# Performance work log

Hardware: AMD Instinct MI355X
Metric: run time of the kernel (lower is better)

## Reference

```python
import jax, jax.numpy as jnp
import numpy as np

HID = 64
NUM_LAYER = 3
N_OBJ = 100000
N_P1, N_P2, N_P3 = 200000, 400000, 200000
NUM_GRAPHS = 256


def _mlp(x, w1, b1, w2, b2):
    # pyg.nn.MLP([in, hid, out], norm=None): Linear -> ReLU -> Linear
    return jnp.dot(jax.nn.relu(jnp.dot(x, w1) + b1), w2) + b2


def _gather(obj, ei):
    # ei: [arity, n_atoms] object index per argument slot
    r, n = ei.shape
    g = jnp.take(obj, ei, axis=0)  # [r, n, HID]
    return jnp.moveaxis(g, 0, 1).reshape(n, r * HID)  # concat per-position embeddings


def _scatter(atom, ei, n_obj):
    # split atom embedding [n, r*HID] into r chunks and scatter-add to objects
    r, n = ei.shape
    chunks = jnp.moveaxis(atom.reshape(n, r, HID), 1, 0).reshape(r * n, HID)
    return jax.ops.segment_sum(chunks, ei.reshape(-1), num_segments=n_obj)


def _lin_init(key, fan_in, fan_out):
    kw, kb = jax.random.split(key)
    w = jax.random.normal(kw, (fan_in, fan_out), jnp.float32) / np.float32(np.sqrt(fan_in))
    b = jax.random.normal(kb, (fan_out,), jnp.float32) * 0.01
    return w, b


def setup_inputs() -> dict:
    key = jax.random.key(0)
    ks = jax.random.split(key, 16)
    inp = {}
    inp["x_obj"] = jnp.zeros((N_OBJ, 1), jnp.float32)
    inp["x_p1"] = jnp.zeros((N_P1, 1), jnp.float32)
    inp["x_p2"] = jnp.zeros((N_P2, 2), jnp.float32)
    inp["x_p3"] = jnp.zeros((N_P3, 3), jnp.float32)
    for i, (name, r) in enumerate([("p1", 1), ("p2", 2), ("p3", 3)]):
        d = HID * r
        w1, b1 = _lin_init(ks[2 * i], d, d)
        w2, b2 = _lin_init(ks[2 * i + 1], d, d)
        inp[f"w_{name}_1"], inp[f"b_{name}_1"] = w1, b1
        inp[f"w_{name}_2"], inp[f"b_{name}_2"] = w2, b2
    inp["w_u1"], inp["b_u1"] = _lin_init(ks[6], 2 * HID, 2 * HID)
    inp["w_u2"], inp["b_u2"] = _lin_init(ks[7], 2 * HID, HID)
    inp["w_r1"], inp["b_r1"] = _lin_init(ks[8], HID, 2 * HID)
    inp["w_r2"], inp["b_r2"] = _lin_init(ks[9], 2 * HID, 1)
    inp["ei_p1"] = jax.random.randint(ks[10], (1, N_P1), 0, N_OBJ, jnp.int32)
    inp["ei_p2"] = jax.random.randint(ks[11], (2, N_P2), 0, N_OBJ, jnp.int32)
    inp["ei_p3"] = jax.random.randint(ks[12], (3, N_P3), 0, N_OBJ, jnp.int32)
    inp["batch_obj"] = jnp.sort(jax.random.randint(ks[13], (N_OBJ,), 0, NUM_GRAPHS, jnp.int32))
    inp["num_graphs"] = NUM_GRAPHS
    return inp


def reference(x_obj, x_p1, x_p2, x_p3,
              w_p1_1, b_p1_1, w_p1_2, b_p1_2,
              w_p2_1, b_p2_1, w_p2_2, b_p2_2,
              w_p3_1, b_p3_1, w_p3_2, b_p3_2,
              w_u1, b_u1, w_u2, b_u2,
              w_r1, b_r1, w_r2, b_r2,
              ei_p1, ei_p2, ei_p3, batch_obj, num_graphs):
    n_obj = x_obj.shape[0]
    # encoding_layer: everything starts at zeros of size [N, F*hidden]
    obj = jnp.zeros((n_obj, x_obj.shape[1] * HID), jnp.float32)
    for _ in range(NUM_LAYER):
        # FanOutMP: gather arg-object embeddings, per-predicate MLP -> atom embeddings
        a1 = _mlp(_gather(obj, ei_p1), w_p1_1, b_p1_1, w_p1_2, b_p1_2)
        a2 = _mlp(_gather(obj, ei_p2), w_p2_1, b_p2_1, w_p2_2, b_p2_2)
        a3 = _mlp(_gather(obj, ei_p3), w_p3_1, b_p3_1, w_p3_2, b_p3_2)
        # FanInMP: split atom emb into arity chunks, scatter-add back to objects
        agg = (_scatter(a1, ei_p1, n_obj) + _scatter(a2, ei_p2, n_obj)
               + _scatter(a3, ei_p3, n_obj))
        # obj_update on cat([old_obj, aggregated])
        obj = _mlp(jnp.concatenate([obj, agg], axis=1), w_u1, b_u1, w_u2, b_u2)
    # global_add_pool + readout
    pooled = jax.ops.segment_sum(obj, batch_obj, num_segments=num_graphs)
    return _mlp(pooled, w_r1, b_r1, w_r2, b_r2).reshape(-1)
```

## Files before the change

### kernel.cpp

```cpp
#include <hip/hip_runtime.h>

typedef _Float16 h8 __attribute__((ext_vector_type(8)));
typedef float f32x4 __attribute__((ext_vector_type(4)));

__device__ __forceinline__ f32x4 mfma2(h8 ah, h8 bh, h8 bl, f32x4 c) {
    c = __builtin_amdgcn_mfma_f32_16x16x32_f16(ah, bh, c, 0, 0, 0);
    c = __builtin_amdgcn_mfma_f32_16x16x32_f16(ah, bl, c, 0, 0, 0);
    return c;
}

__launch_bounds__(256)
__global__ void wprep(const float* __restrict__ w_p1_1, const float* __restrict__ w_p1_2,
                      const float* __restrict__ w_p2_1, const float* __restrict__ w_p2_2,
                      const float* __restrict__ w_p3_1, const float* __restrict__ w_p3_2,
                      const float* __restrict__ w_u1, const float* __restrict__ w_u2,
                      _Float16* __restrict__ hb)
{
    int b = blockIdx.x;
    const float* src; int K, N, base; size_t off;
    if      (b < 16)  { src = w_p1_1; K = 64;  N = 64;  base = 0;   off = 0;      }
    else if (b < 32)  { src = w_p1_2; K = 64;  N = 64;  base = 16;  off = 8192;   }
    else if (b < 96)  { src = w_p2_1; K = 128; N = 128; base = 32;  off = 16384;  }
    else if (b < 160) { src = w_p2_2; K = 128; N = 128; base = 96;  off = 49152;  }
    else if (b < 304) { src = w_p3_1; K = 192; N = 192; base = 160; off = 81920;  }
    else if (b < 448) { src = w_p3_2; K = 192; N = 192; base = 304; off = 155648; }
    else if (b < 512) { src = w_u1;   K = 128; N = 128; base = 448; off = 229376; }
    else              { src = w_u2;   K = 128; N = 64;  base = 512; off = 262144; }
    int e = (b - base) * 256 + threadIdx.x;
    if (e < K * N) {
        int n = e / K, k = e - n * K;
        float x = src[k * N + n];
        _Float16 h = (_Float16)x;
        hb[off + e] = h;
        hb[off + (size_t)K * N + e] = (_Float16)(x - (float)h);
    }
}

__launch_bounds__(256)
__global__ void aconst_k(const float* __restrict__ b_p1_1, const float* __restrict__ w_p1_2,
                         const float* __restrict__ b_p1_2,
                         const float* __restrict__ b_p2_1, const float* __restrict__ w_p2_2,
                         const float* __restrict__ b_p2_2,
                         const float* __restrict__ b_p3_1, const float* __restrict__ w_p3_2,
                         const float* __restrict__ b_p3_2,
                         float* __restrict__ ac)
{
    int p = blockIdx.x;
    const float *b1, *w2, *b2; int D, off;
    if      (p == 0) { b1 = b_p1_1; w2 = w_p1_2; b2 = b_p1_2; D = 64;  off = 0;   }
    else if (p == 1) { b1 = b_p2_1; w2 = w_p2_2; b2 = b_p2_2; D = 128; off = 64;  }
    else             { b1 = b_p3_1; w2 = w_p3_2; b2 = b_p3_2; D = 192; off = 192; }
    int n = threadIdx.x;
    if (n < D) {
        float s = b2[n];
        for (int k = 0; k < D; ++k) {
            float h = b1[k];
            h = h > 0.f ? h : 0.f;
            s = fmaf(h, w2[k * D + n], s);
        }
        ac[off + n] = s;
    }
}

__launch_bounds__(256)
__global__ void hist_k(const int* __restrict__ ei1, const int* __restrict__ ei2,
                       const int* __restrict__ ei3, int* __restrict__ counts,
                       int n_obj, int n1, int n2, int n3)
{
    int e = blockIdx.x * 256 + threadIdx.x;
    int t1 = n1, t2 = n1 + 2 * n2, t3 = t2 + 3 * n3;
    int o, j;
    if (e < t1) { o = ei1[e]; j = 0; }
    else if (e < t2) { int x = e - t1; o = ei2[x]; j = 1 + (x >= n2 ? 1 : 0); }
    else if (e < t3) { int y = e - t2; o = ei3[y]; j = 3 + (y >= n3 ? 1 : 0) + (y >= 2 * n3 ? 1 : 0); }
    else return;
    atomicAdd(&counts[(size_t)j * n_obj + o], 1);
    atomicAdd(&counts[(size_t)6 * n_obj + o], 1);
}

__launch_bounds__(1024)
__global__ void scan_k(const int* __restrict__ deg, int* __restrict__ rowptr,
                       int* __restrict__ cursor, int n)
{
    __shared__ int buf[1024];
    __shared__ int carry_s;
    int tid = threadIdx.x;
    if (tid == 0) carry_s = 0;
    __syncthreads();
    for (int base = 0; base < n; base += 4096) {
        int idx = base + tid * 4;
        int v[4];
#pragma unroll
        for (int k = 0; k < 4; ++k) { int i = idx + k; v[k] = (i < n) ? deg[i] : 0; }
        int tsum = v[0] + v[1] + v[2] + v[3];
        buf[tid] = tsum;
        __syncthreads();
        for (int off = 1; off < 1024; off <<= 1) {
            int t = (tid >= off) ? buf[tid - off] : 0;
            __syncthreads();
            buf[tid] += t;
            __syncthreads();
        }
        int run = buf[tid] - tsum + carry_s;
#pragma unroll
        for (int k = 0; k < 4; ++k) {
            int i = idx + k;
            if (i < n) { rowptr[i] = run; cursor[i] = run; }
            run += v[k];
        }
        __syncthreads();
        if (tid == 1023) carry_s += buf[1023];
        __syncthreads();
    }
    if (tid == 0) rowptr[n] = carry_s;
}

__launch_bounds__(256)
__global__ void fill_k(const int* __restrict__ ei1, const int* __restrict__ ei2,
                       const int* __restrict__ ei3, int* __restrict__ cursor,
                       int* __restrict__ colidx, int n1, int n2, int n3)
{
    int e = blockIdx.x * 256 + threadIdx.x;
    int t1 = n1, t2 = n1 + 2 * n2, t3 = t2 + 3 * n3;
    int o;
    if (e < t1) o = ei1[e];
    else if (e < t2) o = ei2[e - t1];
    else if (e < t3) o = ei3[e - t2];
    else return;
    int pos = atomicAdd(&cursor[o], 1);
    colidx[pos] = e;
}

__launch_bounds__(256)
__global__ void bcast_k(const int* __restrict__ counts, const float* __restrict__ ac,
                        float* __restrict__ agg, int n_obj)
{
    __shared__ float ch[384];
    int tid = threadIdx.x;
    for (int i = tid; i < 384; i += 256) ch[i] = ac[i];
    __syncthreads();
    int i = blockIdx.x * 256 + tid;
    int o = i >> 4, q = i & 15;
    if (o < n_obj) {
        float c[6];
#pragma unroll
        for (int j = 0; j < 6; ++j) c[j] = (float)counts[(size_t)j * n_obj + o];
        float4 v;
        float* vp = (float*)&v;
#pragma unroll
        for (int comp = 0; comp < 4; ++comp) {
            int col = 4 * q + comp;
            float s = 0.f;
#pragma unroll
            for (int j = 0; j < 6; ++j) s = fmaf(c[j], ch[j * 64 + col], s);
            vp[comp] = s;
        }
        ((float4*)agg)[(size_t)o * 16 + q] = v;
    }
}

template<int R, int STORE>
__device__ __forceinline__ void pred_body(
    char* smem,
    const _Float16* __restrict__ objh, const int* __restrict__ ei,
    const _Float16* __restrict__ W1h, const _Float16* __restrict__ W1l,
    const float* __restrict__ B1,
    const _Float16* __restrict__ W2h, const _Float16* __restrict__ W2l,
    const float* __restrict__ B2,
    float* __restrict__ agg, _Float16* __restrict__ chunks, int cbase,
    int n_atoms, int blk)
{
    constexpr int D = 64 * R;
    constexpr int KC = D / 32;
    constexpr int LDA = D + 8;
    _Float16* Ah = (_Float16*)smem;
    int* eis = (int*)(Ah + 64 * LDA);

    const int tid = threadIdx.x;
    const int wave = tid >> 6, lane = tid & 63;
    const int r = lane & 15, g = lane >> 4;
    const int a_base = blk * 64;
    const int tb = wave * R;

    for (int i = tid; i < R * 64; i += 256) {
        int s = i >> 6, a = i & 63;
        int ag = a_base + a; if (ag >= n_atoms) ag = n_atoms - 1;
        eis[i] = ei[s * n_atoms + ag];
    }
    __syncthreads();
    {
        h8 vv[2 * R];
#pragma unroll
        for (int i = 0; i < 2 * R; ++i) {
            int f = tid + 256 * i;
            int rowslot = f >> 3, c = f & 7;
            int s = rowslot >> 6, a = rowslot & 63;
            vv[i] = *(const h8*)(objh + (size_t)eis[s * 64 + a] * 64 + c * 8);
        }
#pragma unroll
        for (int i = 0; i < 2 * R; ++i) {
            int f = tid + 256 * i;
            int rowslot = f >> 3, c = f & 7;
            int s = rowslot >> 6, a = rowslot & 63;
            *(h8*)(Ah + a * LDA + s * 64 + c * 8) = vv[i];
        }
    }
    __syncthreads();

    f32x4 z = {0.f, 0.f, 0.f, 0.f};
    f32x4 acc[4][R];
#pragma unroll
    for (int rt = 0; rt < 4; ++rt)
#pragma unroll
        for (int t = 0; t < R; ++t) acc[rt][t] = z;

    {
        h8 bh[2][R], bl[2][R];
#pragma unroll
        for (int t = 0; t < R; ++t) {
            size_t wo = (size_t)((tb + t) * 16 + r) * D + g * 8;
            bh[0][t] = *(const h8*)(W1h + wo);
            bl[0][t] = *(const h8*)(W1l + wo);
        }
#pragma unroll
        for (int kc = 0; kc < KC; ++kc) {
            const int cur = kc & 1, nxt = cur ^ 1;
            if (kc + 1 < KC) {
#pragma unroll
                for (int t = 0; t < R; ++t) {
                    size_t wo = (size_t)((tb + t) * 16 + r) * D + (kc + 1) * 32 + g * 8;
                    bh[nxt][t] = *(const h8*)(W1h + wo);
                    bl[nxt][t] = *(const h8*)(W1l + wo);
                }
            }
            const int ko = kc * 32 + g * 8;
            h8 ah[4];
#pragma unroll
            for (int rt = 0; rt < 4; ++rt)
                ah[rt] = *(const h8*)(Ah + (rt * 16 + r) * LDA + ko);
#pragma unroll
            for (int t = 0; t < R; ++t)
#pragma unroll
                for (int rt = 0; rt < 4; ++rt)
                    acc[rt][t] = mfma2(ah[rt], bh[cur][t], bl[cur][t], acc[rt][t]);
        }
    }
    __syncthreads();
#pragma unroll
    for (int t = 0; t < R; ++t) {
        int col = (tb + t) * 16 + r;
        float b1 = B1[col];
#pragma unroll
        for (int rt = 0; rt < 4; ++rt)
#pragma unroll
            for (int q = 0; q < 4; ++q) {
                int row = rt * 16 + g * 4 + q;
                float h = acc[rt][t][q] + b1;
                h = h > 0.f ? h : 0.f;
                Ah[row * LDA + col] = (_Float16)h;
            }
    }
    __syncthreads();

#pragma unroll
    for (int rt = 0; rt < 4; ++rt)
#pragma unroll
        for (int t = 0; t < R; ++t) acc[rt][t] = z;
    {
        h8 bh[2][R], bl[2][R];
#pragma unroll
        for (int t = 0; t < R; ++t) {
            size_t wo = (size_t)((tb + t) * 16 + r) * D + g * 8;
            bh[0][t] = *(const h8*)(W2h + wo);
            bl[0][t] = *(const h8*)(W2l + wo);
        }
#pragma unroll
        for (int kc = 0; kc < KC; ++kc) {
            const int cur = kc & 1, nxt = cur ^ 1;
            if (kc + 1 < KC) {
#pragma unroll
                for (int t = 0; t < R; ++t) {
                    size_t wo = (size_t)((tb + t) * 16 + r) * D + (kc + 1) * 32 + g * 8;
                    bh[nxt][t] = *(const h8*)(W2h + wo);
                    bl[nxt][t] = *(const h8*)(W2l + wo);
                }
            }
            const int ko = kc * 32 + g * 8;
            h8 ah[4];
#pragma unroll
            for (int rt = 0; rt < 4; ++rt)
                ah[rt] = *(const h8*)(Ah + (rt * 16 + r) * LDA + ko);
#pragma unroll
            for (int t = 0; t < R; ++t)
#pragma unroll
                for (int rt = 0; rt < 4; ++rt)
                    acc[rt][t] = mfma2(ah[rt], bh[cur][t], bl[cur][t], acc[rt][t]);
        }
    }

#pragma unroll
    for (int t = 0; t < R; ++t) {
        int col = (tb + t) * 16 + r;
        float b2 = B2[col];
        int s = col >> 6, cc = col & 63;
#pragma unroll
        for (int rt = 0; rt < 4; ++rt)
#pragma unroll
            for (int q = 0; q < 4; ++q) {
                int row = rt * 16 + g * 4 + q;
                int atom = a_base + row;
                if (atom < n_atoms) {
                    float v = acc[rt][t][q] + b2;
                    if (STORE) {
                        chunks[(size_t)(cbase + s * n_atoms + atom) * 64 + cc] = (_Float16)v;
                    } else {
                        atomicAdd(agg + (size_t)eis[s * 64 + row] * 64 + cc, v);
                    }
                }
            }
    }
}

template<int STORE>
__launch_bounds__(256, 6)
__global__ void pred_all(const _Float16* __restrict__ objh, float* __restrict__ agg,
                         _Float16* __restrict__ chunks,
                         const int* __restrict__ ei1, const int* __restrict__ ei2,
                         const int* __restrict__ ei3,
                         const _Float16* __restrict__ hb,
                         const float* __restrict__ b_p1_1, const float* __restrict__ b_p1_2,
                         const float* __restrict__ b_p2_1, const float* __restrict__ b_p2_2,
                         const float* __restrict__ b_p3_1, const float* __restrict__ b_p3_2,
                         int n1, int n2, int n3, int nb3, int nb2)
{
    extern __shared__ char smem[];
    int b = blockIdx.x;
    if (b < nb3) {
        pred_body<3, STORE>(smem, objh, ei3, hb + 81920, hb + 118784, b_p3_1,
                            hb + 155648, hb + 192512, b_p3_2, agg, chunks,
                            n1 + 2 * n2, n3, b);
    } else if (b < nb3 + nb2) {
        pred_body<2, STORE>(smem, objh, ei2, hb + 16384, hb + 32768, b_p2_1,
                            hb + 49152, hb + 65536, b_p2_2, agg, chunks,
                            n1, n2, b - nb3);
    } else {
        pred_body<1, STORE>(smem, objh, ei1, hb + 0, hb + 4096, b_p1_1,
                            hb + 8192, hb + 12288, b_p1_2, agg, chunks,
                            0, n1, b - nb3 - nb2);
    }
}

__launch_bounds__(256, 4)
__global__ void fanin_update(_Float16* __restrict__ objh,
                             const _Float16* __restrict__ chunks,
                             const int* __restrict__ rowptr, const int* __restrict__ colidx,
                             const _Float16* __restrict__ W1h, const _Float16* __restrict__ W1l,
                             const float* __restrict__ B1,
                             const _Float16* __restrict__ W2h, const _Float16* __restrict__ W2l,
                             const float* __restrict__ B2,
                             int n_obj, int last, float* __restrict__ aggout)
{
    constexpr int LDA = 136;
    __shared__ _Float16 Ah[64 * LDA];
    __shared__ int cidx[2048];

    const int tid = threadIdx.x;
    const int wave = tid >> 6, lane = tid & 63;
    const int r = lane & 15, g = lane >> 4;
    const int a_base = blockIdx.x * 64;
    const int o_hi = (a_base + 64 < n_obj) ? a_base + 64 : n_obj;

    const int sbeg = rowptr[a_base];
    const int send = rowptr[o_hi];
    const int total = send - sbeg;
    const int ncache = total < 2048 ? total : 2048;
    for (int i = tid; i < ncache; i += 256) cidx[i] = colidx[sbeg + i];

    const int o_local = tid >> 2, part = tid & 3;
    const int o = a_base + o_local;
    const bool valid = o < n_obj;
    const int b = valid ? rowptr[o] : 0;
    const int e2 = valid ? rowptr[o + 1] : 0;
    float s[16];
#pragma unroll
    for (int j = 0; j < 16; ++j) s[j] = 0.f;
    __syncthreads();
    for (int i = b; i < e2; ++i) {
        int li = i - sbeg;
        int row = (li < ncache) ? cidx[li] : colidx[i];
        const h8* cp = (const h8*)(chunks + (size_t)row * 64 + part * 16);
        h8 v0 = cp[0], v1 = cp[1];
#pragma unroll
        for (int j = 0; j < 8; ++j) { s[j] += (float)v0[j]; s[8 + j] += (float)v1[j]; }
    }
    {
        int oc = valid ? o : n_obj - 1;
        h8 u0 = *(const h8*)(objh + (size_t)oc * 64 + part * 16);
        h8 u1 = *(const h8*)(objh + (size_t)oc * 64 + part * 16 + 8);
        *(h8*)(Ah + o_local * LDA + part * 16) = u0;
        *(h8*)(Ah + o_local * LDA + part * 16 + 8) = u1;
        h8 a0, a1;
#pragma unroll
        for (int j = 0; j < 8; ++j) { a0[j] = (_Float16)s[j]; a1[j] = (_Float16)s[8 + j]; }
        *(h8*)(Ah + o_local * LDA + 64 + part * 16) = a0;
        *(h8*)(Ah + o_local * LDA + 64 + part * 16 + 8) = a1;
    }
    __syncthreads();

    f32x4 z = {0.f, 0.f, 0.f, 0.f};
    f32x4 acc[4][2];
#pragma unroll
    for (int rt = 0; rt < 4; ++rt) { acc[rt][0] = z; acc[rt][1] = z; }
    {
        h8 bh[2][2], bl[2][2];
#pragma unroll
        for (int t = 0; t < 2; ++t) {
            size_t wo = (size_t)((wave * 2 + t) * 16 + r) * 128 + g * 8;
            bh[0][t] = *(const h8*)(W1h + wo);
            bl[0][t] = *(const h8*)(W1l + wo);
        }
#pragma unroll
        for (int kc = 0; kc < 4; ++kc) {
            const int cur = kc & 1, nxt = cur ^ 1;
            if (kc + 1 < 4) {
#pragma unroll
                for (int t = 0; t < 2; ++t) {
                    size_t wo = (size_t)((wave * 2 + t) * 16 + r) * 128 + (kc + 1) * 32 + g * 8;
                    bh[nxt][t] = *(const h8*)(W1h + wo);
                    bl[nxt][t] = *(const h8*)(W1l + wo);
                }
            }
            const int ko = kc * 32 + g * 8;
            h8 ah[4];
#pragma unroll
            for (int rt = 0; rt < 4; ++rt)
                ah[rt] = *(const h8*)(Ah + (rt * 16 + r) * LDA + ko);
#pragma unroll
            for (int t = 0; t < 2; ++t)
#pragma unroll
                for (int rt = 0; rt < 4; ++rt)
                    acc[rt][t] = mfma2(ah[rt], bh[cur][t], bl[cur][t], acc[rt][t]);
        }
    }
    __syncthreads();
#pragma unroll
    for (int t = 0; t < 2; ++t) {
        int col = (wave * 2 + t) * 16 + r;
        float b1 = B1[col];
#pragma unroll
        for (int rt = 0; rt < 4; ++rt)
#pragma unroll
            for (int q = 0; q < 4; ++q) {
                int row = rt * 16 + g * 4 + q;
                float h = acc[rt][t][q] + b1;
                h = h > 0.f ? h : 0.f;
                Ah[row * LDA + col] = (_Float16)h;
            }
    }
    __syncthreads();

    f32x4 acc2[4];
#pragma unroll
    for (int rt = 0; rt < 4; ++rt) acc2[rt] = z;
    {
        h8 bh[2], bl[2];
        {
            size_t wo = (size_t)(wave * 16 + r) * 128 + g * 8;
            bh[0] = *(const h8*)(W2h + wo);
            bl[0] = *(const h8*)(W2l + wo);
        }
#pragma unroll
        for (int kc = 0; kc < 4; ++kc) {
            const int cur = kc & 1, nxt = cur ^ 1;
            if (kc + 1 < 4) {
                size_t wo = (size_t)(wave * 16 + r) * 128 + (kc + 1) * 32 + g * 8;
                bh[nxt] = *(const h8*)(W2h + wo);
                bl[nxt] = *(const h8*)(W2l + wo);
            }
            const int ko = kc * 32 + g * 8;
#pragma unroll
            for (int rt = 0; rt < 4; ++rt) {
                h8 ah = *(const h8*)(Ah + (rt * 16 + r) * LDA + ko);
                acc2[rt] = mfma2(ah, bh[cur], bl[cur], acc2[rt]);
            }
        }
    }
    {
        int col = wave * 16 + r;
        float b2 = B2[col];
#pragma unroll
        for (int rt = 0; rt < 4; ++rt)
#pragma unroll
            for (int q = 0; q < 4; ++q) {
                int row = a_base + rt * 16 + g * 4 + q;
                if (row < n_obj) {
                    float v = acc2[rt][q] + b2;
                    if (last) aggout[(size_t)row * 64 + col] = v;
                    else objh[(size_t)row * 64 + col] = (_Float16)v;
                }
            }
    }
}

template<int FIRST>
__launch_bounds__(256, 4)
__global__ void update_mfma(_Float16* __restrict__ objh, float* __restrict__ agg,
                            const _Float16* __restrict__ W1h, const _Float16* __restrict__ W1l,
                            const float* __restrict__ B1,
                            const _Float16* __restrict__ W2h, const _Float16* __restrict__ W2l,
                            const float* __restrict__ B2,
                            int n_obj, int zero_agg, int last)
{
    constexpr int LDA = 136;
    __shared__ _Float16 Ah[64 * LDA];

    const int tid = threadIdx.x;
    const int wave = tid >> 6, lane = tid & 63;
    const int r = lane & 15, g = lane >> 4;
    const int a_base = blockIdx.x * 64;

    {
#pragma unroll
        for (int i = 0; i < 4; ++i) {
            int f = tid + 256 * i;
            int a = f >> 4, c = f & 15;
            int rg = a_base + a; if (rg >= n_obj) rg = n_obj - 1;
            h8 v;
            if (c < 8) {
                if (FIRST) v = (h8)(_Float16)0.f;
                else v = *(const h8*)(objh + (size_t)rg * 64 + c * 8);
            } else {
                float4 f0 = ((const float4*)agg)[(size_t)rg * 16 + (c - 8) * 2];
                float4 f1 = ((const float4*)agg)[(size_t)rg * 16 + (c - 8) * 2 + 1];
                v[0] = (_Float16)f0.x; v[1] = (_Float16)f0.y;
                v[2] = (_Float16)f0.z; v[3] = (_Float16)f0.w;
                v[4] = (_Float16)f1.x; v[5] = (_Float16)f1.y;
                v[6] = (_Float16)f1.z; v[7] = (_Float16)f1.w;
            }
            *(h8*)(Ah + a * LDA + c * 8) = v;
        }
    }
    __syncthreads();

    f32x4 z = {0.f, 0.f, 0.f, 0.f};
    f32x4 acc[4][2];
#pragma unroll
    for (int rt = 0; rt < 4; ++rt) { acc[rt][0] = z; acc[rt][1] = z; }
    {
        h8 bh[2][2], bl[2][2];
#pragma unroll
        for (int t = 0; t < 2; ++t) {
            size_t wo = (size_t)((wave * 2 + t) * 16 + r) * 128 + g * 8;
            bh[0][t] = *(const h8*)(W1h + wo);
            bl[0][t] = *(const h8*)(W1l + wo);
        }
#pragma unroll
        for (int kc = 0; kc < 4; ++kc) {
            const int cur = kc & 1, nxt = cur ^ 1;
            if (kc + 1 < 4) {
#pragma unroll
                for (int t = 0; t < 2; ++t) {
                    size_t wo = (size_t)((wave * 2 + t) * 16 + r) * 128 + (kc + 1) * 32 + g * 8;
                    bh[nxt][t] = *(const h8*)(W1h + wo);
                    bl[nxt][t] = *(const h8*)(W1l + wo);
                }
            }
            const int ko = kc * 32 + g * 8;
            h8 ah[4];
#pragma unroll
            for (int rt = 0; rt < 4; ++rt)
                ah[rt] = *(const h8*)(Ah + (rt * 16 + r) * LDA + ko);
#pragma unroll
            for (int t = 0; t < 2; ++t)
#pragma unroll
                for (int rt = 0; rt < 4; ++rt)
                    acc[rt][t] = mfma2(ah[rt], bh[cur][t], bl[cur][t], acc[rt][t]);
        }
    }
    __syncthreads();
#pragma unroll
    for (int t = 0; t < 2; ++t) {
        int col = (wave * 2 + t) * 16 + r;
        float b1 = B1[col];
#pragma unroll
        for (int rt = 0; rt < 4; ++rt)
#pragma unroll
            for (int q = 0; q < 4; ++q) {
                int row = rt * 16 + g * 4 + q;
                float h = acc[rt][t][q] + b1;
                h = h > 0.f ? h : 0.f;
                Ah[row * LDA + col] = (_Float16)h;
            }
    }
    __syncthreads();

    f32x4 acc2[4];
#pragma unroll
    for (int rt = 0; rt < 4; ++rt) acc2[rt] = z;
    {
        h8 bh[2], bl[2];
        {
            size_t wo = (size_t)(wave * 16 + r) * 128 + g * 8;
            bh[0] = *(const h8*)(W2h + wo);
            bl[0] = *(const h8*)(W2l + wo);
        }
#pragma unroll
        for (int kc = 0; kc < 4; ++kc) {
            const int cur = kc & 1, nxt = cur ^ 1;
            if (kc + 1 < 4) {
                size_t wo = (size_t)(wave * 16 + r) * 128 + (kc + 1) * 32 + g * 8;
                bh[nxt] = *(const h8*)(W2h + wo);
                bl[nxt] = *(const h8*)(W2l + wo);
            }
            const int ko = kc * 32 + g * 8;
#pragma unroll
            for (int rt = 0; rt < 4; ++rt) {
                h8 ah = *(const h8*)(Ah + (rt * 16 + r) * LDA + ko);
                acc2[rt] = mfma2(ah, bh[cur], bl[cur], acc2[rt]);
            }
        }
    }
    __syncthreads();
    {
        int col = wave * 16 + r;
        float b2 = B2[col];
#pragma unroll
        for (int rt = 0; rt < 4; ++rt)
#pragma unroll
            for (int q = 0; q < 4; ++q) {
                int row = a_base + rt * 16 + g * 4 + q;
                if (row < n_obj) {
                    float v = acc2[rt][q] + b2;
                    if (last) agg[(size_t)row * 64 + col] = v;
                    else objh[(size_t)row * 64 + col] = (_Float16)v;
                }
            }
    }
    if (zero_agg) {
        float4 zz = make_float4(0.f, 0.f, 0.f, 0.f);
#pragma unroll
        for (int i = 0; i < 4; ++i) {
            int f = tid + 256 * i;
            int a = f >> 4, q = f & 15;
            int rg = a_base + a;
            if (rg < n_obj) ((float4*)agg)[(size_t)rg * 16 + q] = zz;
        }
    }
}

__global__ void pool_kernel(const float* __restrict__ obj, const int* __restrict__ batch,
                            float* __restrict__ pooled, int n_obj)
{
    int i = blockIdx.x * 256 + threadIdx.x;
    int row = i >> 4, q = i & 15;
    if (row < n_obj) {
        float4 v = ((const float4*)obj)[(size_t)row * 16 + q];
        int g = batch[row];
        float* p = pooled + g * 64 + 4 * q;
        atomicAdd(p + 0, v.x);
        atomicAdd(p + 1, v.y);
        atomicAdd(p + 2, v.z);
        atomicAdd(p + 3, v.w);
    }
}

__launch_bounds__(128)
__global__ void readout_kernel(const float* __restrict__ pooled,
                               const float* __restrict__ w1, const float* __restrict__ b1,
                               const float* __restrict__ w2, const float* __restrict__ b2,
                               float* __restrict__ out)
{
    int g = blockIdx.x, c = threadIdx.x;
    __shared__ float xs[64];
    __shared__ float red[2];
    if (c < 64) xs[c] = pooled[g * 64 + c];
    __syncthreads();
    float h = b1[c];
#pragma unroll
    for (int k = 0; k < 64; ++k) h = fmaf(xs[k], w1[k * 128 + c], h);
    float v = fmaxf(h, 0.f) * w2[c];
#pragma unroll
    for (int off = 32; off > 0; off >>= 1) v += __shfl_down(v, off);
    if ((c & 63) == 0) red[c >> 6] = v;
    __syncthreads();
    if (c == 0) out[g] = red[0] + red[1] + b2[0];
}

static inline size_t align_up(size_t x) { return (x + 255) & ~(size_t)255; }

extern "C" void kernel_launch(void* const* d_in, const int* in_sizes, int n_in,
                              void* d_out, int out_size, void* d_ws, size_t ws_size,
                              hipStream_t stream)
{
    const float* w_p1_1 = (const float*)d_in[4];
    const float* b_p1_1 = (const float*)d_in[5];
    const float* w_p1_2 = (const float*)d_in[6];
    const float* b_p1_2 = (const float*)d_in[7];
    const float* w_p2_1 = (const float*)d_in[8];
    const float* b_p2_1 = (const float*)d_in[9];
    const float* w_p2_2 = (const float*)d_in[10];
    const float* b_p2_2 = (const float*)d_in[11];
    const float* w_p3_1 = (const float*)d_in[12];
    const float* b_p3_1 = (const float*)d_in[13];
    const float* w_p3_2 = (const float*)d_in[14];
    const float* b_p3_2 = (const float*)d_in[15];
    const float* w_u1 = (const float*)d_in[16];
    const float* b_u1 = (const float*)d_in[17];
    const float* w_u2 = (const float*)d_in[18];
    const float* b_u2 = (const float*)d_in[19];
    const float* w_r1 = (const float*)d_in[20];
    const float* b_r1 = (const float*)d_in[21];
    const float* w_r2 = (const float*)d_in[22];
    const float* b_r2 = (const float*)d_in[23];
    const int* ei_p1 = (const int*)d_in[24];
    const int* ei_p2 = (const int*)d_in[25];
    const int* ei_p3 = (const int*)d_in[26];
    const int* batch = (const int*)d_in[27];

    const int n_obj = in_sizes[0];
    const int n_p1 = in_sizes[24];
    const int n_p2 = in_sizes[25] / 2;
    const int n_p3 = in_sizes[26] / 3;
    const int E = n_p1 + 2 * n_p2 + 3 * n_p3;

    char* base = (char*)d_ws;
    size_t off = 0;
    _Float16* objh = (_Float16*)(base + off); off = align_up(off + (size_t)n_obj * 64 * 2);
    float* agg = (float*)(base + off);        off = align_up(off + (size_t)n_obj * 64 * 4);
    float* pooled = (float*)(base + off);     off = align_up(off + (size_t)out_size * 64 * 4);
    _Float16* hb = (_Float16*)(base + off);   off = align_up(off + (size_t)278528 * 2);
    int* counts = (int*)(base + off);         off = align_up(off + (size_t)7 * n_obj * 4);
    int* deg = counts + (size_t)6 * n_obj;
    int* rowptr = (int*)(base + off);         off = align_up(off + ((size_t)n_obj + 1) * 4);
    int* cursor = (int*)(base + off);         off = align_up(off + (size_t)n_obj * 4);
    int* colidx = (int*)(base + off);         off = align_up(off + (size_t)E * 4);
    _Float16* chunks = (_Float16*)(base + off); off = align_up(off + (size_t)E * 64 * 2);
    const bool csr_ok = off <= ws_size;

    const int nb3 = (n_p3 + 63) / 64, nb2 = (n_p2 + 63) / 64, nb1 = (n_p1 + 63) / 64;
    const int pred_smem = 64 * (192 + 8) * 2 + 3 * 64 * 4;

    wprep<<<544, 256, 0, stream>>>(w_p1_1, w_p1_2, w_p2_1, w_p2_2, w_p3_1, w_p3_2,
                                   w_u1, w_u2, hb);
    aconst_k<<<3, 256, 0, stream>>>(b_p1_1, w_p1_2, b_p1_2, b_p2_1, w_p2_2, b_p2_2,
                                    b_p3_1, w_p3_2, b_p3_2, agg);
    float* ac = pooled;
    aconst_k<<<3, 256, 0, stream>>>(b_p1_1, w_p1_2, b_p1_2, b_p2_1, w_p2_2, b_p2_2,
                                    b_p3_1, w_p3_2, b_p3_2, ac);
    hipMemsetAsync(counts, 0, (size_t)7 * n_obj * sizeof(int), stream);
    hist_k<<<(E + 255) / 256, 256, 0, stream>>>(ei_p1, ei_p2, ei_p3, counts,
                                                n_obj, n_p1, n_p2, n_p3);
    if (csr_ok) {
        scan_k<<<1, 1024, 0, stream>>>(deg, rowptr, cursor, n_obj);
        fill_k<<<(E + 255) / 256, 256, 0, stream>>>(ei_p1, ei_p2, ei_p3, cursor, colidx,
                                                    n_p1, n_p2, n_p3);
    }
    bcast_k<<<((size_t)n_obj * 16 + 255) / 256, 256, 0, stream>>>(counts, ac, agg, n_obj);
    update_mfma<1><<<(n_obj + 63) / 64, 256, 0, stream>>>(
        objh, agg, hb + 229376, hb + 245760, b_u1, hb + 262144, hb + 270336, b_u2,
        n_obj, csr_ok ? 0 : 1, 0);
    if (csr_ok) {
        for (int l = 1; l < 3; ++l) {
            pred_all<1><<<nb3 + nb2 + nb1, 256, pred_smem, stream>>>(
                objh, agg, chunks, ei_p1, ei_p2, ei_p3, hb,
                b_p1_1, b_p1_2, b_p2_1, b_p2_2, b_p3_1, b_p3_2,
                n_p1, n_p2, n_p3, nb3, nb2);
            fanin_update<<<(n_obj + 63) / 64, 256, 0, stream>>>(
                objh, chunks, rowptr, colidx,
                hb + 229376, hb + 245760, b_u1, hb + 262144, hb + 270336, b_u2,
                n_obj, l == 2 ? 1 : 0, agg);
        }
    } else {
        for (int l = 1; l < 3; ++l) {
            pred_all<0><<<nb3 + nb2 + nb1, 256, pred_smem, stream>>>(
                objh, agg, chunks, ei_p1, ei_p2, ei_p3, hb,
                b_p1_1, b_p1_2, b_p2_1, b_p2_2, b_p3_1, b_p3_2,
                n_p1, n_p2, n_p3, nb3, nb2);
            update_mfma<0><<<(n_obj + 63) / 64, 256, 0, stream>>>(
                objh, agg, hb + 229376, hb + 245760, b_u1, hb + 262144, hb + 270336, b_u2,
                n_obj, l < 2 ? 1 : 0, l == 2 ? 1 : 0);
        }
    }
    hipMemsetAsync(pooled, 0, (size_t)out_size * 64 * sizeof(float), stream);
    pool_kernel<<<((size_t)n_obj * 16 + 255) / 256, 256, 0, stream>>>(agg, batch, pooled, n_obj);
    readout_kernel<<<out_size, 128, 0, stream>>>(pooled, w_r1, b_r1, w_r2, b_r2, (float*)d_out);
}
```

Before: 1.469 ms.

## Scatter atom chunks directly into CSR order and store aggregate in fp16

fill_k now records each edge's destination slot in the CSR order. The predicate kernel stages its outputs in shared memory and writes each 64-wide chunk straight to that slot, so fanin_update reads contiguous chunks with no colidx indirection or index caching. The aggregate buffer becomes fp16, with half2 atomics in the fallback path and h8 loads in the update kernel, which halves traffic. In exchange, the chunk writes become scattered and extra syncthreads are added, and fp16 accumulation in the fallback loses precision.

```diff
diff --git a/kernel.cpp b/kernel.cpp
--- a/kernel.cpp
+++ b/kernel.cpp
@@ -1,4 +1,5 @@
 #include <hip/hip_runtime.h>
+#include <hip/hip_fp16.h>
 
 typedef _Float16 h8 __attribute__((ext_vector_type(8)));
 typedef float f32x4 __attribute__((ext_vector_type(4)));
@@ -118,7 +119,7 @@
 __launch_bounds__(256)
 __global__ void fill_k(const int* __restrict__ ei1, const int* __restrict__ ei2,
                        const int* __restrict__ ei3, int* __restrict__ cursor,
-                       int* __restrict__ colidx, int n1, int n2, int n3)
+                       int* __restrict__ epos, int n1, int n2, int n3)
 {
     int e = blockIdx.x * 256 + threadIdx.x;
     int t1 = n1, t2 = n1 + 2 * n2, t3 = t2 + 3 * n3;
@@ -127,35 +128,33 @@
     else if (e < t2) o = ei2[e - t1];
     else if (e < t3) o = ei3[e - t2];
     else return;
-    int pos = atomicAdd(&cursor[o], 1);
-    colidx[pos] = e;
+    epos[e] = atomicAdd(&cursor[o], 1);
 }
 
 __launch_bounds__(256)
 __global__ void bcast_k(const int* __restrict__ counts, const float* __restrict__ ac,
-                        float* __restrict__ agg, int n_obj)
+                        _Float16* __restrict__ aggh, int n_obj)
 {
     __shared__ float ch[384];
     int tid = threadIdx.x;
     for (int i = tid; i < 384; i += 256) ch[i] = ac[i];
     __syncthreads();
     int i = blockIdx.x * 256 + tid;
-    int o = i >> 4, q = i & 15;
+    int o = i >> 3, q = i & 7;
     if (o < n_obj) {
         float c[6];
 #pragma unroll
         for (int j = 0; j < 6; ++j) c[j] = (float)counts[(size_t)j * n_obj + o];
-        float4 v;
-        float* vp = (float*)&v;
-#pragma unroll
-        for (int comp = 0; comp < 4; ++comp) {
-            int col = 4 * q + comp;
+        h8 v;
+#pragma unroll
+        for (int comp = 0; comp < 8; ++comp) {
+            int col = 8 * q + comp;
             float s = 0.f;
 #pragma unroll
             for (int j = 0; j < 6; ++j) s = fmaf(c[j], ch[j * 64 + col], s);
-            vp[comp] = s;
-        }
-        ((float4*)agg)[(size_t)o * 16 + q] = v;
+            v[comp] = (_Float16)s;
+        }
+        *(h8*)(aggh + (size_t)o * 64 + 8 * q) = v;
     }
 }
 
@@ -163,11 +162,12 @@
 __device__ __forceinline__ void pred_body(
     char* smem,
     const _Float16* __restrict__ objh, const int* __restrict__ ei,
+    const int* __restrict__ epos, int cbase,
     const _Float16* __restrict__ W1h, const _Float16* __restrict__ W1l,
     const float* __restrict__ B1,
     const _Float16* __restrict__ W2h, const _Float16* __restrict__ W2l,
     const float* __restrict__ B2,
-    float* __restrict__ agg, _Float16* __restrict__ chunks, int cbase,
+    _Float16* __restrict__ aggh, _Float16* __restrict__ chunks,
     int n_atoms, int blk)
 {
     constexpr int D = 64 * R;
@@ -298,33 +298,61 @@
         }
     }
 
-#pragma unroll
-    for (int t = 0; t < R; ++t) {
-        int col = (tb + t) * 16 + r;
-        float b2 = B2[col];
-        int s = col >> 6, cc = col & 63;
-#pragma unroll
-        for (int rt = 0; rt < 4; ++rt)
-#pragma unroll
-            for (int q = 0; q < 4; ++q) {
-                int row = rt * 16 + g * 4 + q;
-                int atom = a_base + row;
-                if (atom < n_atoms) {
+    if (STORE) {
+        __syncthreads();
+#pragma unroll
+        for (int t = 0; t < R; ++t) {
+            int col = (tb + t) * 16 + r;
+            float b2 = B2[col];
+            int s = col >> 6, cc = col & 63;
+#pragma unroll
+            for (int rt = 0; rt < 4; ++rt)
+#pragma unroll
+                for (int q = 0; q < 4; ++q) {
+                    int row = rt * 16 + g * 4 + q;
+                    Ah[row * LDA + s * 64 + cc] = (_Float16)(acc[rt][t][q] + b2);
+                }
+        }
+        __syncthreads();
+#pragma unroll
+        for (int p = 0; p < 2 * R; ++p) {
+            int i = p * 32 + (tid >> 3);
+            int s = i >> 6, a = i & 63;
+            int c8 = tid & 7;
+            int atom = a_base + a;
+            if (atom < n_atoms) {
+                int pos = epos[cbase + s * n_atoms + atom];
+                *(h8*)(chunks + (size_t)pos * 64 + c8 * 8) =
+                    *(const h8*)(Ah + a * LDA + s * 64 + c8 * 8);
+            }
+        }
+    } else {
+#pragma unroll
+        for (int t = 0; t < R; ++t) {
+            int col = (tb + t) * 16 + r;
+            float b2 = B2[col];
+            int s = col >> 6, cc = col & 63;
+#pragma unroll
+            for (int rt = 0; rt < 4; ++rt)
+#pragma unroll
+                for (int q = 0; q < 4; ++q) {
+                    int row = rt * 16 + g * 4 + q;
+                    int atom = a_base + row;
                     float v = acc[rt][t][q] + b2;
-                    if (STORE) {
-                        chunks[(size_t)(cbase + s * n_atoms + atom) * 64 + cc] = (_Float16)v;
-                    } else {
-                        atomicAdd(agg + (size_t)eis[s * 64 + row] * 64 + cc, v);
+                    float v2 = __shfl_xor(v, 1);
+                    if (atom < n_atoms && (r & 1) == 0) {
+                        __half2 hv = __floats2half2_rn(v, v2);
+                        unsafeAtomicAdd((__half2*)(aggh + (size_t)eis[s * 64 + row] * 64 + cc), hv);
                     }
                 }
-            }
+        }
     }
 }
 
 template<int STORE>
 __launch_bounds__(256, 6)
-__global__ void pred_all(const _Float16* __restrict__ objh, float* __restrict__ agg,
-                         _Float16* __restrict__ chunks,
+__global__ void pred_all(const _Float16* __restrict__ objh, _Float16* __restrict__ aggh,
+                         _Float16* __restrict__ chunks, const int* __restrict__ epos,
                          const int* __restrict__ ei1, const int* __restrict__ ei2,
                          const int* __restrict__ ei3,
                          const _Float16* __restrict__ hb,
@@ -336,45 +364,37 @@
     extern __shared__ char smem[];
     int b = blockIdx.x;
     if (b < nb3) {
-        pred_body<3, STORE>(smem, objh, ei3, hb + 81920, hb + 118784, b_p3_1,
-                            hb + 155648, hb + 192512, b_p3_2, agg, chunks,
-                            n1 + 2 * n2, n3, b);
+        pred_body<3, STORE>(smem, objh, ei3, epos, n1 + 2 * n2,
+                            hb + 81920, hb + 118784, b_p3_1,
+                            hb + 155648, hb + 192512, b_p3_2, aggh, chunks, n3, b);
     } else if (b < nb3 + nb2) {
-        pred_body<2, STORE>(smem, objh, ei2, hb + 16384, hb + 32768, b_p2_1,
-                            hb + 49152, hb + 65536, b_p2_2, agg, chunks,
-                            n1, n2, b - nb3);
+        pred_body<2, STORE>(smem, objh, ei2, epos, n1,
+                            hb + 16384, hb + 32768, b_p2_1,
+                            hb + 49152, hb + 65536, b_p2_2, aggh, chunks, n2, b - nb3);
     } else {
-        pred_body<1, STORE>(smem, objh, ei1, hb + 0, hb + 4096, b_p1_1,
-                            hb + 8192, hb + 12288, b_p1_2, agg, chunks,
-                            0, n1, b - nb3 - nb2);
+        pred_body<1, STORE>(smem, objh, ei1, epos, 0,
+                            hb + 0, hb + 4096, b_p1_1,
+                            hb + 8192, hb + 12288, b_p1_2, aggh, chunks, n1, b - nb3 - nb2);
     }
 }
 
 __launch_bounds__(256, 4)
 __global__ void fanin_update(_Float16* __restrict__ objh,
                              const _Float16* __restrict__ chunks,
-                             const int* __restrict__ rowptr, const int* __restrict__ colidx,
+                             const int* __restrict__ rowptr,
                              const _Float16* __restrict__ W1h, const _Float16* __restrict__ W1l,
                              const float* __restrict__ B1,
                              const _Float16* __restrict__ W2h, const _Float16* __restrict__ W2l,
                              const float* __restrict__ B2,
-                             int n_obj, int last, float* __restrict__ aggout)
+                             int n_obj, int last, float* __restrict__ aggf)
 {
     constexpr int LDA = 136;
     __shared__ _Float16 Ah[64 * LDA];
-    __shared__ int cidx[2048];
 
     const int tid = threadIdx.x;
     const int wave = tid >> 6, lane = tid & 63;
     const int r = lane & 15, g = lane >> 4;
     const int a_base = blockIdx.x * 64;
-    const int o_hi = (a_base + 64 < n_obj) ? a_base + 64 : n_obj;
-
-    const int sbeg = rowptr[a_base];
-    const int send = rowptr[o_hi];
-    const int total = send - sbeg;
-    const int ncache = total < 2048 ? total : 2048;
-    for (int i = tid; i < ncache; i += 256) cidx[i] = colidx[sbeg + i];
 
     const int o_local = tid >> 2, part = tid & 3;
     const int o = a_base + o_local;
@@ -384,11 +404,8 @@
     float s[16];
 #pragma unroll
     for (int j = 0; j < 16; ++j) s[j] = 0.f;
-    __syncthreads();
     for (int i = b; i < e2; ++i) {
-        int li = i - sbeg;
-        int row = (li < ncache) ? cidx[li] : colidx[i];
-        const h8* cp = (const h8*)(chunks + (size_t)row * 64 + part * 16);
+        const h8* cp = (const h8*)(chunks + (size_t)i * 64 + part * 16);
         h8 v0 = cp[0], v1 = cp[1];
 #pragma unroll
         for (int j = 0; j < 8; ++j) { s[j] += (float)v0[j]; s[8 + j] += (float)v1[j]; }
@@ -495,7 +512,7 @@
                 int row = a_base + rt * 16 + g * 4 + q;
                 if (row < n_obj) {
                     float v = acc2[rt][q] + b2;
-                    if (last) aggout[(size_t)row * 64 + col] = v;
+                    if (last) aggf[(size_t)row * 64 + col] = v;
                     else objh[(size_t)row * 64 + col] = (_Float16)v;
                 }
             }
@@ -504,12 +521,12 @@
 
 template<int FIRST>
 __launch_bounds__(256, 4)
-__global__ void update_mfma(_Float16* __restrict__ objh, float* __restrict__ agg,
+__global__ void update_mfma(_Float16* __restrict__ objh, _Float16* __restrict__ aggh,
                             const _Float16* __restrict__ W1h, const _Float16* __restrict__ W1l,
                             const float* __restrict__ B1,
                             const _Float16* __restrict__ W2h, const _Float16* __restrict__ W2l,
                             const float* __restrict__ B2,
-                            int n_obj, int zero_agg, int last)
+                            int n_obj, int zero_agg, int last, float* __restrict__ aggf)
 {
     constexpr int LDA = 136;
     __shared__ _Float16 Ah[64 * LDA];
@@ -530,12 +547,7 @@
                 if (FIRST) v = (h8)(_Float16)0.f;
                 else v = *(const h8*)(objh + (size_t)rg * 64 + c * 8);
             } else {
-                float4 f0 = ((const float4*)agg)[(size_t)rg * 16 + (c - 8) * 2];
-                float4 f1 = ((const float4*)agg)[(size_t)rg * 16 + (c - 8) * 2 + 1];
-                v[0] = (_Float16)f0.x; v[1] = (_Float16)f0.y;
-                v[2] = (_Float16)f0.z; v[3] = (_Float16)f0.w;
-                v[4] = (_Float16)f1.x; v[5] = (_Float16)f1.y;
-                v[6] = (_Float16)f1.z; v[7] = (_Float16)f1.w;
+                v = *(const h8*)(aggh + (size_t)rg * 64 + (c - 8) * 8);
             }
             *(h8*)(Ah + a * LDA + c * 8) = v;
         }
@@ -631,19 +643,19 @@
                 int row = a_base + rt * 16 + g * 4 + q;
                 if (row < n_obj) {
                     float v = acc2[rt][q] + b2;
-                    if (last) agg[(size_t)row * 64 + col] = v;
+                    if (last) aggf[(size_t)row * 64 + col] = v;
                     else objh[(size_t)row * 64 + col] = (_Float16)v;
                 }
             }
     }
     if (zero_agg) {
-        float4 zz = make_float4(0.f, 0.f, 0.f, 0.f);
-#pragma unroll
-        for (int i = 0; i < 4; ++i) {
+        h8 zz = (h8)(_Float16)0.f;
+#pragma unroll
+        for (int i = 0; i < 2; ++i) {
             int f = tid + 256 * i;
-            int a = f >> 4, q = f & 15;
+            int a = f >> 3, q = f & 7;
             int rg = a_base + a;
-            if (rg < n_obj) ((float4*)agg)[(size_t)rg * 16 + q] = zz;
+            if (rg < n_obj) *(h8*)(aggh + (size_t)rg * 64 + q * 8) = zz;
         }
     }
 }
@@ -726,25 +738,24 @@
     char* base = (char*)d_ws;
     size_t off = 0;
     _Float16* objh = (_Float16*)(base + off); off = align_up(off + (size_t)n_obj * 64 * 2);
-    float* agg = (float*)(base + off);        off = align_up(off + (size_t)n_obj * 64 * 4);
+    _Float16* aggh = (_Float16*)(base + off); off = align_up(off + (size_t)n_obj * 64 * 2);
+    float* aggf = (float*)(base + off);       off = align_up(off + (size_t)n_obj * 64 * 4);
     float* pooled = (float*)(base + off);     off = align_up(off + (size_t)out_size * 64 * 4);
     _Float16* hb = (_Float16*)(base + off);   off = align_up(off + (size_t)278528 * 2);
     int* counts = (int*)(base + off);         off = align_up(off + (size_t)7 * n_obj * 4);
     int* deg = counts + (size_t)6 * n_obj;
     int* rowptr = (int*)(base + off);         off = align_up(off + ((size_t)n_obj + 1) * 4);
     int* cursor = (int*)(base + off);         off = align_up(off + (size_t)n_obj * 4);
-    int* colidx = (int*)(base + off);         off = align_up(off + (size_t)E * 4);
+    int* epos = (int*)(base + off);           off = align_up(off + (size_t)E * 4);
     _Float16* chunks = (_Float16*)(base + off); off = align_up(off + (size_t)E * 64 * 2);
     const bool csr_ok = off <= ws_size;
+    float* ac = pooled;
 
     const int nb3 = (n_p3 + 63) / 64, nb2 = (n_p2 + 63) / 64, nb1 = (n_p1 + 63) / 64;
     const int pred_smem = 64 * (192 + 8) * 2 + 3 * 64 * 4;
 
     wprep<<<544, 256, 0, stream>>>(w_p1_1, w_p1_2, w_p2_1, w_p2_2, w_p3_1, w_p3_2,
                                    w_u1, w_u2, hb);
-    aconst_k<<<3, 256, 0, stream>>>(b_p1_1, w_p1_2, b_p1_2, b_p2_1, w_p2_2, b_p2_2,
-                                    b_p3_1, w_p3_2, b_p3_2, agg);
-    float* ac = pooled;
     aconst_k<<<3, 256, 0, stream>>>(b_p1_1, w_p1_2, b_p1_2, b_p2_1, w_p2_2, b_p2_2,
                                     b_p3_1, w_p3_2, b_p3_2, ac);
     hipMemsetAsync(counts, 0, (size_t)7 * n_obj * sizeof(int), stream);
@@ -752,36 +763,36 @@
                                                 n_obj, n_p1, n_p2, n_p3);
     if (csr_ok) {
         scan_k<<<1, 1024, 0, stream>>>(deg, rowptr, cursor, n_obj);
-        fill_k<<<(E + 255) / 256, 256, 0, stream>>>(ei_p1, ei_p2, ei_p3, cursor, colidx,
+        fill_k<<<(E + 255) / 256, 256, 0, stream>>>(ei_p1, ei_p2, ei_p3, cursor, epos,
                                                     n_p1, n_p2, n_p3);
     }
-    bcast_k<<<((size_t)n_obj * 16 + 255) / 256, 256, 0, stream>>>(counts, ac, agg, n_obj);
+    bcast_k<<<((size_t)n_obj * 8 + 255) / 256, 256, 0, stream>>>(counts, ac, aggh, n_obj);
     update_mfma<1><<<(n_obj + 63) / 64, 256, 0, stream>>>(
-        objh, agg, hb + 229376, hb + 245760, b_u1, hb + 262144, hb + 270336, b_u2,
-        n_obj, csr_ok ? 0 : 1, 0);
+        objh, aggh, hb + 229376, hb + 245760, b_u1, hb + 262144, hb + 270336, b_u2,
+        n_obj, csr_ok ? 0 : 1, 0, aggf);
     if (csr_ok) {
         for (int l = 1; l < 3; ++l) {
             pred_all<1><<<nb3 + nb2 + nb1, 256, pred_smem, stream>>>(
-                objh, agg, chunks, ei_p1, ei_p2, ei_p3, hb,
+                objh, aggh, chunks, epos, ei_p1, ei_p2, ei_p3, hb,
                 b_p1_1, b_p1_2, b_p2_1, b_p2_2, b_p3_1, b_p3_2,
                 n_p1, n_p2, n_p3, nb3, nb2);
             fanin_update<<<(n_obj + 63) / 64, 256, 0, stream>>>(
-                objh, chunks, rowptr, colidx,
+                objh, chunks, rowptr,
                 hb + 229376, hb + 245760, b_u1, hb + 262144, hb + 270336, b_u2,
-                n_obj, l == 2 ? 1 : 0, agg);
+                n_obj, l == 2 ? 1 : 0, aggf);
         }
     } else {
         for (int l = 1; l < 3; ++l) {
             pred_all<0><<<nb3 + nb2 + nb1, 256, pred_smem, stream>>>(
-                objh, agg, chunks, ei_p1, ei_p2, ei_p3, hb,
+                objh, aggh, chunks, epos, ei_p1, ei_p2, ei_p3, hb,
                 b_p1_1, b_p1_2, b_p2_1, b_p2_2, b_p3_1, b_p3_2,
                 n_p1, n_p2, n_p3, nb3, nb2);
             update_mfma<0><<<(n_obj + 63) / 64, 256, 0, stream>>>(
-                objh, agg, hb + 229376, hb + 245760, b_u1, hb + 262144, hb + 270336, b_u2,
-                n_obj, l < 2 ? 1 : 0, l == 2 ? 1 : 0);
+                objh, aggh, hb + 229376, hb + 245760, b_u1, hb + 262144, hb + 270336, b_u2,
+                n_obj, l < 2 ? 1 : 0, l == 2 ? 1 : 0, aggf);
         }
     }
     hipMemsetAsync(pooled, 0, (size_t)out_size * 64 * sizeof(float), stream);
-    pool_kernel<<<((size_t)n_obj * 16 + 255) / 256, 256, 0, stream>>>(agg, batch, pooled, n_obj);
+    pool_kernel<<<((size_t)n_obj * 16 + 255) / 256, 256, 0, stream>>>(aggf, batch, pooled, n_obj);
     readout_kernel<<<out_size, 128, 0, stream>>>(pooled, w_r1, b_r1, w_r2, b_r2, (float*)d_out);
 }
```

Result: faster. 1.416 ms (-3.6%).
